# Kernel tuning notes

Measured on AMD Instinct MI355X. Metric: run time of the kernel, lower is better.

## Reference

```python
import jax, jax.numpy as jnp
import numpy as np

H, W, C = 96, 96, 21
SIGMA_RGB = 3.0   # bilateral spatial sdims (as called in the original code)
SIGMA_XY = 64.0   # gaussian spatial sdims
SCHAN = 255.0     # bilateral color std
COMPAT = 10.0     # Potts compatibility weight (same for both kernels)
N_ITERS = 5


def _gauss_kernel(feats):
    # feats: [N, D] -> K[i,j] = exp(-0.5 * ||f_i - f_j||^2)
    sq = jnp.sum(feats * feats, axis=-1)
    d2 = sq[:, None] + sq[None, :] - 2.0 * (feats @ feats.T)
    return jnp.exp(-0.5 * jnp.maximum(d2, 0.0))


def setup_inputs() -> dict:
    key = jax.random.key(0)
    k1, k2, k3 = jax.random.split(key, 3)
    logits = jax.random.normal(k1, (1, C, H, W), dtype=jnp.float32)
    labels = jax.random.randint(k2, (1, H, W), 0, C, dtype=jnp.int32)
    image = jax.random.uniform(k3, (1, 3, H, W), dtype=jnp.float32) * 255.0
    return {"logits": logits, "labels": labels, "image": image, "num_classes": C}


def reference(logits, labels, image, num_classes):
    # unary potentials: U = -log_softmax(logits)
    logp = jax.nn.log_softmax(logits, axis=1)              # [1,C,H,W]
    U = (-logp)[0].reshape(num_classes, -1).T              # [N,C]

    # pixel features
    yy, xx = jnp.meshgrid(jnp.arange(H), jnp.arange(W), indexing="ij")
    pos = jnp.stack([yy, xx], axis=-1).reshape(-1, 2).astype(logits.dtype)  # [N,2]
    rgb = image[0].transpose(1, 2, 0).reshape(-1, 3)        # [N,3]

    # dense pairwise kernels (exact Gaussian / bilateral, self-connection removed)
    N = H * W
    eye = jnp.eye(N, dtype=logits.dtype)
    Kg = _gauss_kernel(pos / SIGMA_XY) - eye
    fb = jnp.concatenate([pos / SIGMA_RGB, rgb / SCHAN], axis=-1)
    Kb = _gauss_kernel(fb) - eye

    # mean-field inference, Potts compatibility mu(l,l') = [l != l']
    Q0 = jax.nn.softmax(-U, axis=1)                         # [N,C]

    def step(Q, _):
        msg = Kg @ Q + Kb @ Q                               # [N,C] filtered Q
        pair = COMPAT * (jnp.sum(msg, axis=1, keepdims=True) - msg)
        Q = jax.nn.softmax(-U - pair, axis=1)
        return Q, None

    Q, _ = jax.lax.scan(step, Q0, None, length=N_ITERS)
    pairwise = Q.T.reshape(1, num_classes, H, W)

    # cross entropy (mean over pixels)
    ce = -jnp.mean(jnp.take_along_axis(logp, labels[:, None].astype(jnp.int32), axis=1))

    return ce + pairwise                                    # broadcast, as in original
```

## Files before the change

kernel.cpp:

```cpp
#include <hip/hip_runtime.h>
#include <hip/hip_fp16.h>

#define HH 96
#define WW 96
#define CC 21
#define NN (HH*WW)
#define NBLK (NN/256)
#define STRIDE 24
#define ROWF (WW*STRIDE)
#define NRUN (NN/8)
#define NTILE 576

typedef _Float16 f16x8 __attribute__((ext_vector_type(8)));
typedef float f32x4 __attribute__((ext_vector_type(4)));

union H8 { f16x8 v; __half2 h2[4]; };


__global__ __launch_bounds__(256) void k_setup(
    const float* __restrict__ logits, const int* __restrict__ labels,
    const float* __restrict__ image, float* __restrict__ U,
    float* __restrict__ Q0, _Float16* __restrict__ QTa,
    _Float16* __restrict__ QTb, float* __restrict__ gtab,
    float* __restrict__ partial) {
  const int t = threadIdx.x;
  const int i = blockIdx.x * 256 + t;
  const int qoff = (i >> 3) * 192 + (i & 7);

  float d[CC];
  float mx = -1e30f;
#pragma unroll
  for (int c = 0; c < CC; ++c) {
    d[c] = logits[c * NN + i];
    mx = fmaxf(mx, d[c]);
  }
  float s = 0.f;
#pragma unroll
  for (int c = 0; c < CC; ++c) { d[c] -= mx; s += __expf(d[c]); }
  const float lse = logf(s);
  const float inv = 1.f / s;
  const int lab = labels[i];
  float myU = 0.f;
#pragma unroll
  for (int c = 0; c < CC; ++c) {
    const float Uc = lse - d[c];
    const float q = __expf(d[c]) * inv;
    U[i * STRIDE + c] = Uc;
    Q0[i * STRIDE + c] = q;
    QTa[qoff + c * 8] = (_Float16)q;
    myU = (c == lab) ? Uc : myU;
  }
  const float rr = image[i] * (1.f / 255.f);
  const float rg = image[NN + i] * (1.f / 255.f);
  const float rb = image[2 * NN + i] * (1.f / 255.f);
  U[i * STRIDE + 21] = 0.f;
  U[i * STRIDE + 22] = 0.f;
  U[i * STRIDE + 23] = 0.f;
  Q0[i * STRIDE + 21] = rr;
  Q0[i * STRIDE + 22] = rg;
  Q0[i * STRIDE + 23] = rb;
  QTa[qoff + 21 * 8] = (_Float16)rr;
  QTa[qoff + 22 * 8] = (_Float16)rg;
  QTa[qoff + 23 * 8] = (_Float16)rb;
  QTb[qoff + 21 * 8] = (_Float16)rr;
  QTb[qoff + 22 * 8] = (_Float16)rg;
  QTb[qoff + 23 * 8] = (_Float16)rb;

  if (blockIdx.x == 0 && t < 96) {
    const float dv = (float)t * (1.f / 64.f);
    gtab[t] = __expf(-0.5f * dv * dv);
  }

  __shared__ float red[256];
  red[t] = myU;
  __syncthreads();
  for (int off = 128; off > 0; off >>= 1) {
    if (t < off) red[t] += red[t + off];
    __syncthreads();
  }
  if (t == 0) partial[blockIdx.x] = red[0];
}

__global__ __launch_bounds__(256) void k_gauss_y(
    const float* __restrict__ Qin, float* __restrict__ Gy,
    const float* __restrict__ gtab) {
  __shared__ float g[96];
  if (threadIdx.x < 96) g[threadIdx.x] = gtab[threadIdx.x];
  __syncthreads();
  const int idx = blockIdx.x * 256 + threadIdx.x;
  const int y = idx / ROWF;
  const int rem = idx - y * ROWF;
  const float* base = Qin + rem;
  float a0 = 0.f, a1 = 0.f, a2 = 0.f, a3 = 0.f;
#pragma unroll 6
  for (int yp = 0; yp < HH; yp += 4) {
    a0 = fmaf(g[abs(y - yp)], base[yp * ROWF], a0);
    a1 = fmaf(g[abs(y - yp - 1)], base[(yp + 1) * ROWF], a1);
    a2 = fmaf(g[abs(y - yp - 2)], base[(yp + 2) * ROWF], a2);
    a3 = fmaf(g[abs(y - yp - 3)], base[(yp + 3) * ROWF], a3);
  }
  Gy[idx] = (a0 + a1) + (a2 + a3);
}

__global__ __launch_bounds__(256) void k_gauss_x(
    const float* __restrict__ Gy, float* __restrict__ G,
    const float* __restrict__ gtab) {
  __shared__ float g[96];
  if (threadIdx.x < 96) g[threadIdx.x] = gtab[threadIdx.x];
  __syncthreads();
  const int idx = blockIdx.x * 256 + threadIdx.x;
  const int y = idx / ROWF;
  const int rem = idx - y * ROWF;
  const int x = rem / STRIDE;
  const int c = rem - x * STRIDE;
  const float* base = Gy + y * ROWF + c;
  float a0 = 0.f, a1 = 0.f, a2 = 0.f, a3 = 0.f;
#pragma unroll 6
  for (int xp = 0; xp < WW; xp += 4) {
    a0 = fmaf(g[abs(x - xp)], base[xp * STRIDE], a0);
    a1 = fmaf(g[abs(x - xp - 1)], base[(xp + 1) * STRIDE], a1);
    a2 = fmaf(g[abs(x - xp - 2)], base[(xp + 2) * STRIDE], a2);
    a3 = fmaf(g[abs(x - xp - 3)], base[(xp + 3) * STRIDE], a3);
  }
  G[idx] = (a0 + a1) + (a2 + a3);
}

__global__ __launch_bounds__(512) void k_bilat(
    const float* __restrict__ U, const float* __restrict__ Qin,
    const float* __restrict__ G, const _Float16* __restrict__ QT,
    float* __restrict__ Qout, _Float16* __restrict__ QTout,
    const float* __restrict__ partial, float* __restrict__ out, int last) {
  __shared__ __half sytab[64];
  __shared__ __half2 sxtab[64];
  __shared__ float psum[8][16][24];
  __shared__ float sces;

  const int tid = threadIdx.x;
  const int w = tid >> 6;
  const int l = tid & 63;
  const int g = l >> 4;
  const int q = l & 15;

  if (tid < 64) {
    const float dv = (float)(tid - 32);
    sytab[tid] = __float2half(__expf(dv * dv * (-1.f / 18.f)));
    const float dv1 = dv + 1.f;
    sxtab[tid] = __floats2half2_rn(__expf(dv * dv * (-1.f / 18.f)),
                                   __expf(dv1 * dv1 * (-1.f / 18.f)));
    if (last) {
      float v = (tid < NBLK) ? partial[tid] : 0.f;
#pragma unroll
      for (int off = 32; off >= 1; off >>= 1) v += __shfl_xor(v, off, 64);
      if (tid == 0) sces = v * (1.f / (float)NN);
    }
  }
  __syncthreads();

  const int tile = blockIdx.x;
  const int ty0 = (tile / 24) * 4;
  const int tx0 = (tile - (tile / 24) * 24) * 4;

  const int pr = q >> 2, pc = q & 3;
  const int yi = ty0 + pr, xi = tx0 + pc;
  const int ipix = yi * WW + xi;

  const float4 rown = *(const float4*)(Qin + ipix * STRIDE + 20);
  const __half2 ri_r = __float2half2_rn(rown.y);
  const __half2 ri_g = __float2half2_rn(rown.z);
  const __half2 ri_b = __float2half2_rn(rown.w);
  const __half2 mhalf = __floats2half2_rn(-0.5f, -0.5f);
  const __half hzero = __float2half(0.f);

  const int xs = tx0 - 16;
  const int xbase0 = (xs > 0 ? xs : 0) & ~7;
  const int rid0 = (w < 4) ? w * 23 : 92 + (w - 4) * 22;
  const int nrun = (w < 4) ? 23 : 22;
  const int row2 = (16 + q > 23) ? 23 : 16 + q;

  f32x4 acc0 = {0.f, 0.f, 0.f, 0.f};
  f32x4 acc1 = {0.f, 0.f, 0.f, 0.f};

#pragma unroll
  for (int ck = 0; ck < 6; ++ck) {
    const int r = ck * 4 + g;
    const int rid = rid0 + r;
    const int wr = rid / 5;
    const int cs = rid - wr * 5;
    const int yj = ty0 - 16 + wr;
    const int xb = xbase0 + cs * 8;
    const bool ok = (r < nrun) & (yj >= 0) & (yj < HH) & (xb <= WW - 8);
    const int yc = min(max(yj, 0), HH - 1);
    const int xc = min(xb, WW - 8);
    const _Float16* base = QT + (yc * 12 + (xc >> 3)) * 192;

    H8 b1, b2, rj, gj, bj;
    b1.v = *(const f16x8*)(base + q * 8);
    b2.v = *(const f16x8*)(base + row2 * 8);
    rj.v = *(const f16x8*)(base + 21 * 8);
    gj.v = *(const f16x8*)(base + 22 * 8);
    bj.v = *(const f16x8*)(base + 23 * 8);

    const int dy = yj - yi;
    const int iy = min(max(dy + 32, 0), 63);
    const __half syv = ok ? sytab[iy] : hzero;
    const __half2 sy2 = __half2half2(syv);
    const int dx0 = xb - xi;
    const int ix0 = min(max(dx0 + 32, 0), 57);

    H8 af;
#pragma unroll
    for (int e2 = 0; e2 < 4; ++e2) {
      const __half2 sx2 = sxtab[ix0 + 2 * e2];
      const __half2 dr = __hsub2(rj.h2[e2], ri_r);
      const __half2 dg = __hsub2(gj.h2[e2], ri_g);
      const __half2 db = __hsub2(bj.h2[e2], ri_b);
      __half2 d2c = __hmul2(dr, dr);
      d2c = __hfma2(dg, dg, d2c);
      d2c = __hfma2(db, db, d2c);
      const __half2 ec = h2exp(__hmul2(d2c, mhalf));
      af.h2[e2] = __hmul2(__hmul2(sy2, sx2), ec);
    }
    acc0 = __builtin_amdgcn_mfma_f32_16x16x32_f16(af.v, b1.v, acc0, 0, 0, 0);
    acc1 = __builtin_amdgcn_mfma_f32_16x16x32_f16(af.v, b2.v, acc1, 0, 0, 0);
  }

#pragma unroll
  for (int reg = 0; reg < 4; ++reg) {
    psum[w][g * 4 + reg][q] = acc0[reg];
    if (q < 8) psum[w][g * 4 + reg][16 + q] = acc1[reg];
  }
  __syncthreads();

  const int half_ = l >> 5;
  const int cl = l & 31;
  const bool act = cl < CC;
  const int pix = w * 2 + half_;
  const int py = ty0 + (pix >> 2), px = tx0 + (pix & 3);
  const int ip = py * WW + px;
  float Qic = 0.f;
  if (cl < STRIDE) Qic = Qin[ip * STRIDE + cl];
  float tcv = 0.f, Uc = 0.f, Gc = 0.f;
  if (act) {
    tcv = psum[0][pix][cl] + psum[1][pix][cl] + psum[2][pix][cl] +
          psum[3][pix][cl] + psum[4][pix][cl] + psum[5][pix][cl] +
          psum[6][pix][cl] + psum[7][pix][cl];
    Uc = U[ip * STRIDE + cl];
    Gc = G[ip * STRIDE + cl];
  }
  const float contrib = act ? (tcv + Gc - 2.f * Qic) : 0.f;
  float tot = contrib;
#pragma unroll
  for (int off = 16; off >= 1; off >>= 1) tot += __shfl_xor(tot, off, 32);
  const float lc = act ? (-Uc - 10.f * (tot - contrib)) : -1e30f;
  float mxl = lc;
#pragma unroll
  for (int off = 16; off >= 1; off >>= 1)
    mxl = fmaxf(mxl, __shfl_xor(mxl, off, 32));
  const float e = act ? __expf(lc - mxl) : 0.f;
  float se = e;
#pragma unroll
  for (int off = 16; off >= 1; off >>= 1) se += __shfl_xor(se, off, 32);
  const float qnew = e / se;
  if (last) {
    if (act) out[cl * NN + ip] = sces + qnew;
  } else {
    if (cl < STRIDE) Qout[ip * STRIDE + cl] = act ? qnew : Qic;
    if (act) QTout[(ip >> 3) * 192 + cl * 8 + (ip & 7)] = (_Float16)qnew;
  }
}

extern "C" void kernel_launch(void* const* d_in, const int* in_sizes, int n_in,
                              void* d_out, int out_size, void* d_ws,
                              size_t ws_size, hipStream_t stream) {
  const float* logits = (const float*)d_in[0];
  const int* labels = (const int*)d_in[1];
  const float* image = (const float*)d_in[2];
  float* ws = (float*)d_ws;

  float* U = ws;
  float* Qa = U + NN * STRIDE;
  float* Qb = Qa + NN * STRIDE;
  float* Gy = Qb + NN * STRIDE;
  float* G = Gy + NN * STRIDE;
  float* gtab = G + NN * STRIDE;
  float* partial = gtab + 96;
  float* cepad = partial + 64;
  _Float16* QTa = (_Float16*)(cepad + 64);
  _Float16* QTb = QTa + NRUN * 192;

  k_setup<<<NBLK, 256, 0, stream>>>(logits, labels, image, U, Qa, QTa, QTb,
                                    gtab, partial);

  const float* qi = Qa;
  float* qo = Qb;
  const _Float16* qti = QTa;
  _Float16* qto = QTb;
  const int gblk = NN * STRIDE / 256;
  for (int it = 0; it < 5; ++it) {
    k_gauss_y<<<gblk, 256, 0, stream>>>(qi, Gy, gtab);
    k_gauss_x<<<gblk, 256, 0, stream>>>(Gy, G, gtab);
    k_bilat<<<NTILE, 512, 0, stream>>>(U, qi, G, qti, qo, qto, partial,
                                       (float*)d_out, it == 4);
    qi = qo;
    qo = (qo == Qb) ? Qa : Qb;
    const _Float16* tmp = qti;
    qti = qto;
    qto = (_Float16*)tmp;
  }
}
```

Measured before the change: 137.7 us.

## Fuse separable Gaussian passes into one kernel and halve bilateral block waves

Merges the y and x passes of the separable Gaussian filter into one kernel with one block per image row. The y-filtered row stays in shared memory, and the weight table is computed inside the kernel, which removes one launch per iteration and the Gy round trip through global memory. The bilateral kernel drops from 8 waves to 4 per tile, each wave covering twice as many neighbour runs, and each half-wave now finalises two pixels. The cost is only 96 blocks for the Gaussian work, which may underfill the GPU, and fewer waves per tile with less latency hiding in the bilateral pass.

```diff
diff --git a/kernel.cpp b/kernel.cpp
--- a/kernel.cpp
+++ b/kernel.cpp
@@ -21,8 +21,7 @@
     const float* __restrict__ logits, const int* __restrict__ labels,
     const float* __restrict__ image, float* __restrict__ U,
     float* __restrict__ Q0, _Float16* __restrict__ QTa,
-    _Float16* __restrict__ QTb, float* __restrict__ gtab,
-    float* __restrict__ partial) {
+    _Float16* __restrict__ QTb, float* __restrict__ partial) {
   const int t = threadIdx.x;
   const int i = blockIdx.x * 256 + t;
   const int qoff = (i >> 3) * 192 + (i & 7);
@@ -66,11 +65,6 @@
   QTb[qoff + 22 * 8] = (_Float16)rg;
   QTb[qoff + 23 * 8] = (_Float16)rb;
 
-  if (blockIdx.x == 0 && t < 96) {
-    const float dv = (float)t * (1.f / 64.f);
-    gtab[t] = __expf(-0.5f * dv * dv);
-  }
-
   __shared__ float red[256];
   red[t] = myU;
   __syncthreads();
@@ -81,58 +75,65 @@
   if (t == 0) partial[blockIdx.x] = red[0];
 }
 
-__global__ __launch_bounds__(256) void k_gauss_y(
-    const float* __restrict__ Qin, float* __restrict__ Gy,
-    const float* __restrict__ gtab) {
+__global__ __launch_bounds__(1024) void k_gauss(
+    const float* __restrict__ Qin, float* __restrict__ G) {
+  __shared__ float sGy[ROWF];
   __shared__ float g[96];
-  if (threadIdx.x < 96) g[threadIdx.x] = gtab[threadIdx.x];
-  __syncthreads();
-  const int idx = blockIdx.x * 256 + threadIdx.x;
-  const int y = idx / ROWF;
-  const int rem = idx - y * ROWF;
-  const float* base = Qin + rem;
-  float a0 = 0.f, a1 = 0.f, a2 = 0.f, a3 = 0.f;
+
+  const int tid = threadIdx.x;
+  const int y = blockIdx.x;
+  if (tid < 96) {
+    const float dv = (float)tid * (1.f / 64.f);
+    g[tid] = __expf(-0.5f * dv * dv);
+  }
+  __syncthreads();
+
+#pragma unroll
+  for (int k = 0; k < 3; ++k) {
+    const int p = tid + (k << 10);
+    if (p < ROWF) {
+      const float* col = Qin + p;
+      float a0 = 0.f, a1 = 0.f, a2 = 0.f, a3 = 0.f;
 #pragma unroll 6
-  for (int yp = 0; yp < HH; yp += 4) {
-    a0 = fmaf(g[abs(y - yp)], base[yp * ROWF], a0);
-    a1 = fmaf(g[abs(y - yp - 1)], base[(yp + 1) * ROWF], a1);
-    a2 = fmaf(g[abs(y - yp - 2)], base[(yp + 2) * ROWF], a2);
-    a3 = fmaf(g[abs(y - yp - 3)], base[(yp + 3) * ROWF], a3);
-  }
-  Gy[idx] = (a0 + a1) + (a2 + a3);
+      for (int yp = 0; yp < HH; yp += 4) {
+        a0 = fmaf(g[abs(y - yp)], col[yp * ROWF], a0);
+        a1 = fmaf(g[abs(y - yp - 1)], col[(yp + 1) * ROWF], a1);
+        a2 = fmaf(g[abs(y - yp - 2)], col[(yp + 2) * ROWF], a2);
+        a3 = fmaf(g[abs(y - yp - 3)], col[(yp + 3) * ROWF], a3);
+      }
+      sGy[p] = (a0 + a1) + (a2 + a3);
+    }
+  }
+  __syncthreads();
+
+#pragma unroll
+  for (int k = 0; k < 3; ++k) {
+    const int p = tid + (k << 10);
+    if (p < ROWF) {
+      const int x = p / STRIDE;
+      const int c = p - x * STRIDE;
+      const float* base = sGy + c;
+      float a0 = 0.f, a1 = 0.f, a2 = 0.f, a3 = 0.f;
+#pragma unroll 6
+      for (int xp = 0; xp < WW; xp += 4) {
+        a0 = fmaf(g[abs(x - xp)], base[xp * STRIDE], a0);
+        a1 = fmaf(g[abs(x - xp - 1)], base[(xp + 1) * STRIDE], a1);
+        a2 = fmaf(g[abs(x - xp - 2)], base[(xp + 2) * STRIDE], a2);
+        a3 = fmaf(g[abs(x - xp - 3)], base[(xp + 3) * STRIDE], a3);
+      }
+      G[y * ROWF + p] = (a0 + a1) + (a2 + a3);
+    }
+  }
 }
 
-__global__ __launch_bounds__(256) void k_gauss_x(
-    const float* __restrict__ Gy, float* __restrict__ G,
-    const float* __restrict__ gtab) {
-  __shared__ float g[96];
-  if (threadIdx.x < 96) g[threadIdx.x] = gtab[threadIdx.x];
-  __syncthreads();
-  const int idx = blockIdx.x * 256 + threadIdx.x;
-  const int y = idx / ROWF;
-  const int rem = idx - y * ROWF;
-  const int x = rem / STRIDE;
-  const int c = rem - x * STRIDE;
-  const float* base = Gy + y * ROWF + c;
-  float a0 = 0.f, a1 = 0.f, a2 = 0.f, a3 = 0.f;
-#pragma unroll 6
-  for (int xp = 0; xp < WW; xp += 4) {
-    a0 = fmaf(g[abs(x - xp)], base[xp * STRIDE], a0);
-    a1 = fmaf(g[abs(x - xp - 1)], base[(xp + 1) * STRIDE], a1);
-    a2 = fmaf(g[abs(x - xp - 2)], base[(xp + 2) * STRIDE], a2);
-    a3 = fmaf(g[abs(x - xp - 3)], base[(xp + 3) * STRIDE], a3);
-  }
-  G[idx] = (a0 + a1) + (a2 + a3);
-}
-
-__global__ __launch_bounds__(512) void k_bilat(
+__global__ __launch_bounds__(256) void k_bilat(
     const float* __restrict__ U, const float* __restrict__ Qin,
     const float* __restrict__ G, const _Float16* __restrict__ QT,
     float* __restrict__ Qout, _Float16* __restrict__ QTout,
     const float* __restrict__ partial, float* __restrict__ out, int last) {
   __shared__ __half sytab[64];
   __shared__ __half2 sxtab[64];
-  __shared__ float psum[8][16][24];
+  __shared__ float psum[4][16][24];
   __shared__ float sces;
 
   const int tid = threadIdx.x;
@@ -173,22 +174,21 @@
 
   const int xs = tx0 - 16;
   const int xbase0 = (xs > 0 ? xs : 0) & ~7;
-  const int rid0 = (w < 4) ? w * 23 : 92 + (w - 4) * 22;
-  const int nrun = (w < 4) ? 23 : 22;
+  const int rid0 = w * 45;
   const int row2 = (16 + q > 23) ? 23 : 16 + q;
 
   f32x4 acc0 = {0.f, 0.f, 0.f, 0.f};
   f32x4 acc1 = {0.f, 0.f, 0.f, 0.f};
 
 #pragma unroll
-  for (int ck = 0; ck < 6; ++ck) {
+  for (int ck = 0; ck < 12; ++ck) {
     const int r = ck * 4 + g;
     const int rid = rid0 + r;
     const int wr = rid / 5;
     const int cs = rid - wr * 5;
     const int yj = ty0 - 16 + wr;
     const int xb = xbase0 + cs * 8;
-    const bool ok = (r < nrun) & (yj >= 0) & (yj < HH) & (xb <= WW - 8);
+    const bool ok = (r < 45) & (yj >= 0) & (yj < HH) & (xb <= WW - 8);
     const int yc = min(max(yj, 0), HH - 1);
     const int xc = min(xb, WW - 8);
     const _Float16* base = QT + (yc * 12 + (xc >> 3)) * 192;
@@ -234,38 +234,40 @@
   const int half_ = l >> 5;
   const int cl = l & 31;
   const bool act = cl < CC;
-  const int pix = w * 2 + half_;
-  const int py = ty0 + (pix >> 2), px = tx0 + (pix & 3);
-  const int ip = py * WW + px;
-  float Qic = 0.f;
-  if (cl < STRIDE) Qic = Qin[ip * STRIDE + cl];
-  float tcv = 0.f, Uc = 0.f, Gc = 0.f;
-  if (act) {
-    tcv = psum[0][pix][cl] + psum[1][pix][cl] + psum[2][pix][cl] +
-          psum[3][pix][cl] + psum[4][pix][cl] + psum[5][pix][cl] +
-          psum[6][pix][cl] + psum[7][pix][cl];
-    Uc = U[ip * STRIDE + cl];
-    Gc = G[ip * STRIDE + cl];
-  }
-  const float contrib = act ? (tcv + Gc - 2.f * Qic) : 0.f;
-  float tot = contrib;
-#pragma unroll
-  for (int off = 16; off >= 1; off >>= 1) tot += __shfl_xor(tot, off, 32);
-  const float lc = act ? (-Uc - 10.f * (tot - contrib)) : -1e30f;
-  float mxl = lc;
-#pragma unroll
-  for (int off = 16; off >= 1; off >>= 1)
-    mxl = fmaxf(mxl, __shfl_xor(mxl, off, 32));
-  const float e = act ? __expf(lc - mxl) : 0.f;
-  float se = e;
-#pragma unroll
-  for (int off = 16; off >= 1; off >>= 1) se += __shfl_xor(se, off, 32);
-  const float qnew = e / se;
-  if (last) {
-    if (act) out[cl * NN + ip] = sces + qnew;
-  } else {
-    if (cl < STRIDE) Qout[ip * STRIDE + cl] = act ? qnew : Qic;
-    if (act) QTout[(ip >> 3) * 192 + cl * 8 + (ip & 7)] = (_Float16)qnew;
+#pragma unroll
+  for (int p2 = 0; p2 < 2; ++p2) {
+    const int pix = (w << 2) + (half_ << 1) + p2;
+    const int py = ty0 + (pix >> 2), px = tx0 + (pix & 3);
+    const int ip = py * WW + px;
+    float Qic = 0.f;
+    if (cl < STRIDE) Qic = Qin[ip * STRIDE + cl];
+    float tcv = 0.f, Uc = 0.f, Gc = 0.f;
+    if (act) {
+      tcv = psum[0][pix][cl] + psum[1][pix][cl] + psum[2][pix][cl] +
+            psum[3][pix][cl];
+      Uc = U[ip * STRIDE + cl];
+      Gc = G[ip * STRIDE + cl];
+    }
+    const float contrib = act ? (tcv + Gc - 2.f * Qic) : 0.f;
+    float tot = contrib;
+#pragma unroll
+    for (int off = 16; off >= 1; off >>= 1) tot += __shfl_xor(tot, off, 32);
+    const float lc = act ? (-Uc - 10.f * (tot - contrib)) : -1e30f;
+    float mxl = lc;
+#pragma unroll
+    for (int off = 16; off >= 1; off >>= 1)
+      mxl = fmaxf(mxl, __shfl_xor(mxl, off, 32));
+    const float e = act ? __expf(lc - mxl) : 0.f;
+    float se = e;
+#pragma unroll
+    for (int off = 16; off >= 1; off >>= 1) se += __shfl_xor(se, off, 32);
+    const float qnew = e / se;
+    if (last) {
+      if (act) out[cl * NN + ip] = sces + qnew;
+    } else {
+      if (cl < STRIDE) Qout[ip * STRIDE + cl] = act ? qnew : Qic;
+      if (act) QTout[(ip >> 3) * 192 + cl * 8 + (ip & 7)] = (_Float16)qnew;
+    }
   }
 }
 
@@ -280,26 +282,22 @@
   float* U = ws;
   float* Qa = U + NN * STRIDE;
   float* Qb = Qa + NN * STRIDE;
-  float* Gy = Qb + NN * STRIDE;
-  float* G = Gy + NN * STRIDE;
-  float* gtab = G + NN * STRIDE;
-  float* partial = gtab + 96;
+  float* G = Qb + NN * STRIDE;
+  float* partial = G + NN * STRIDE;
   float* cepad = partial + 64;
   _Float16* QTa = (_Float16*)(cepad + 64);
   _Float16* QTb = QTa + NRUN * 192;
 
   k_setup<<<NBLK, 256, 0, stream>>>(logits, labels, image, U, Qa, QTa, QTb,
-                                    gtab, partial);
+                                    partial);
 
   const float* qi = Qa;
   float* qo = Qb;
   const _Float16* qti = QTa;
   _Float16* qto = QTb;
-  const int gblk = NN * STRIDE / 256;
   for (int it = 0; it < 5; ++it) {
-    k_gauss_y<<<gblk, 256, 0, stream>>>(qi, Gy, gtab);
-    k_gauss_x<<<gblk, 256, 0, stream>>>(Gy, G, gtab);
-    k_bilat<<<NTILE, 512, 0, stream>>>(U, qi, G, qti, qo, qto, partial,
+    k_gauss<<<HH, 1024, 0, stream>>>(qi, G);
+    k_bilat<<<NTILE, 256, 0, stream>>>(U, qi, G, qti, qo, qto, partial,
                                        (float*)d_out, it == 4);
     qi = qo;
     qo = (qo == Qb) ? Qa : Qb;
```

After: 178.4 us. 1.3x slower.
